# Performance work log

Hardware: AMD Instinct MI355X
Metric: run time of the kernel (lower is better)

The kernel has to match this reference:

```python
import jax, jax.numpy as jnp
from jax import lax
import numpy as np

# (in_ch, out_ch, kernel) per SparseConv layer; last layer has no ReLU
LAYERS = [(1, 16, 11), (16, 16, 7), (16, 16, 5), (16, 16, 3), (16, 16, 3), (16, 1, 1)]
DN = ('NCHW', 'OIHW', 'NCHW')


def _sparse_conv(x, mask, w, bias, gamma, beta, relu):
    k = w.shape[-1]
    p = k // 2
    pad = [(p, p), (p, p)]
    xm = x * mask  # mask broadcasts over channels ([B,1,H,W])
    y = lax.conv_general_dilated(xm, w, (1, 1), pad, dimension_numbers=DN)
    # 'sparsity' conv: fixed all-ones [1,1,k,k] kernel over the 1-channel mask
    ones_k = jnp.ones((1, 1, k, k), x.dtype)
    s = lax.conv_general_dilated(mask, ones_k, (1, 1), pad, dimension_numbers=DN)
    y = y * (1.0 / (s + 1e-8)) + bias[None, :, None, None]
    # BatchNorm2d in training mode (batch statistics), eps=1e-5
    mean = jnp.mean(y, axis=(0, 2, 3), keepdims=True)
    var = jnp.var(y, axis=(0, 2, 3), keepdims=True)
    y = (y - mean) * lax.rsqrt(var + 1e-5)
    y = y * gamma[None, :, None, None] + beta[None, :, None, None]
    if relu:
        y = jnp.maximum(y, 0.0)
    # MaxPool2d(k, stride=1, padding=k//2) on the mask (pads with -inf)
    mask = lax.reduce_window(mask, -jnp.inf, lax.max, (1, 1, k, k), (1, 1, 1, 1),
                             [(0, 0), (0, 0), (p, p), (p, p)])
    return y, mask


def setup_inputs() -> dict:
    key = jax.random.key(0)
    kx, *kws = jax.random.split(key, 1 + len(LAYERS))
    inp = {"x": jax.random.uniform(kx, (4, 2, 1024, 1024), dtype=jnp.float32)}
    for i, (cin, cout, k) in enumerate(LAYERS, start=1):
        fan_in = cin * k * k
        inp[f"w{i}"] = jax.random.normal(kws[i - 1], (cout, cin, k, k), jnp.float32) / np.sqrt(fan_in)
        inp[f"b{i}"] = jnp.zeros((cout,), jnp.float32)
        inp[f"g{i}"] = jnp.ones((cout,), jnp.float32)
        inp[f"bt{i}"] = jnp.zeros((cout,), jnp.float32)
    return inp


def reference(x, w1, b1, g1, bt1, w2, b2, g2, bt2, w3, b3, g3, bt3,
              w4, b4, g4, bt4, w5, b5, g5, bt5, w6, b6, g6, bt6):
    data = x[:, 0:1]   # channels != 1 (input_channels=2 -> channel 0)
    mask = x[:, 1:2]   # channel 1
    params = [(w1, b1, g1, bt1), (w2, b2, g2, bt2), (w3, b3, g3, bt3),
              (w4, b4, g4, bt4), (w5, b5, g5, bt5), (w6, b6, g6, bt6)]
    h, m = data, mask
    for i, (w, b, g, bt) in enumerate(params):
        h, m = _sparse_conv(h, m, w, b, g, bt, relu=(i < 5))
    return h
```

## Files before the change

kernel.cpp:

```cpp
#include <hip/hip_runtime.h>
#include <hip/hip_bf16.h>


#define HW (1024 * 1024)
typedef __hip_bfloat16 bf16;
typedef __attribute__((ext_vector_type(8))) short s8v;
typedef __attribute__((ext_vector_type(4))) float f4v;

__device__ __forceinline__ float b2f(bf16 v) { return __bfloat162float(v); }
__device__ __forceinline__ bf16  f2b(float v) { return __float2bfloat16(v); }
__device__ __forceinline__ short fbits(float v) {
    bf16 t = f2b(v); short s; __builtin_memcpy(&s, &t, 2); return s;
}
__device__ __forceinline__ float bs2f(short s) {
    bf16 t; __builtin_memcpy(&t, &s, 2); return __bfloat162float(t);
}

__device__ __forceinline__ float ldv(const void* p, int i, bool isf) {
    return isf ? ((const float*)p)[i] : b2f(((const bf16*)p)[i]);
}

__device__ __forceinline__ float wave_reduce(float v) {
    #pragma unroll
    for (int off = 32; off > 0; off >>= 1)
        v += __shfl_down(v, off, 64);
    return v;
}

__global__ void probeKernel(const unsigned short* __restrict__ xb,
                            float* __restrict__ stats)
{
    __shared__ int sbad;
    const int tid = threadIdx.x;
    if (tid == 0) sbad = 0;
    __syncthreads();
    int bad = 0;
    for (int i = tid; i < 4096; i += 256) {
        unsigned u = ((unsigned)xb[i]) << 16;
        float v = __uint_as_float(u);
        if (!(v >= 0.f && v < 1.f)) bad = 1;
    }
    if (bad) sbad = 1;
    __syncthreads();
    if (tid == 0) stats[380] = sbad ? 1.f : 0.f;
}

__global__ void transposeW1(const void* __restrict__ w, bf16* __restrict__ wb,
                            const float* flagp)
{
    const bool isf = (*flagp > 0.5f);
    int j = blockIdx.x * 256 + threadIdx.x;
    if (j < 3072) {
        int col8 = j & 7;
        int co = (j >> 3) & 15;
        int k8 = j >> 7;
        int k = k8 * 8 + col8;
        int dy = k >> 4, dx = k & 15;
        float v = (dy < 11 && dx < 11) ? ldv(w, co * 121 + dy * 11 + dx, isf) : 0.f;
        wb[j] = f2b(v);
    }
}

__global__ void transposeWB(const void* __restrict__ w, bf16* __restrict__ wtB,
                            int KK, int NT, const float* flagp)
{
    const bool isf = (*flagp > 0.5f);
    int j = blockIdx.x * 256 + threadIdx.x;
    if (j < NT * 256) {
        int t = j >> 8, co = (j >> 4) & 15, c = j & 15;
        float v = (t < KK) ? ldv(w, (co * 16 + c) * KK + t, isf) : 0.f;
        wtB[j] = f2b(v);
    }
}

template <int TM, int TK, int WP>
__device__ __forceinline__ void buildMaskTile(
    const void* __restrict__ mask0, bool isf, float* sm0, float* vm,
    float* mprev, int bx, int by, int tid)
{
    constexpr int H1 = (TM - 32) / 2;
    constexpr int H2 = (TK - 32) / 2;
    for (int i = tid; i < TM * TM; i += 256) {
        int yy = by - H1 + i / TM, xx = bx - H1 + i % TM;
        float m = 0.f;
        if ((unsigned)yy < 1024u && (unsigned)xx < 1024u)
            m = ldv(mask0, (yy << 10) + xx, isf);
        sm0[i] = m;
    }
    __syncthreads();
    for (int i = tid; i < TK * TM; i += 256) {
        int y = i / TM, xc = i % TM;
        float mx = 0.f;
        for (int d = 0; d < WP; ++d) mx = fmaxf(mx, sm0[(y + d) * TM + xc]);
        vm[i] = mx;
    }
    __syncthreads();
    for (int i = tid; i < TK * TK; i += 256) {
        int y = i / TK, xc = i % TK;
        int gy = by - H2 + y, gx = bx - H2 + xc;
        float mx = 0.f;
        if ((unsigned)gy < 1024u && (unsigned)gx < 1024u)
            for (int d = 0; d < WP; ++d) mx = fmaxf(mx, vm[y * TM + xc + d]);
        mprev[i] = mx;
    }
    __syncthreads();
}

__device__ __forceinline__ const void* maskChanPtr(const void* x, int n, bool isf) {
    return isf ? (const void*)((const float*)x + n * 2 * HW + HW)
               : (const void*)((const bf16*)x + n * 2 * HW + HW);
}

__global__ __launch_bounds__(256) void convFirstM(
    const void* __restrict__ x, const bf16* __restrict__ wb1,
    const void* __restrict__ bias, bf16* __restrict__ out,
    float* statsCur, const float* flagp)
{
    constexpr int ST = 48, ROWS = 44, MT = 42;
    __shared__ alignas(16) short c0[ROWS * ST];
    __shared__ alignas(16) short c1[ROWS * ST + 2];
    __shared__ float smask[MT * MT];
    __shared__ float scs[32 * MT];
    __shared__ float sinv[1024];
    __shared__ float red[128];
    const bool isf = (*flagp > 0.5f);
    const int n = blockIdx.z;
    const int bx = blockIdx.x * 32, by = blockIdx.y * 32;
    const int tid = threadIdx.x, lane = tid & 63, wid = tid >> 6;
    const int nn = lane & 15, q = lane >> 4;

    s8v Bf[6];
    #pragma unroll
    for (int kb = 0; kb < 6; ++kb)
        Bf[kb] = *(const s8v*)(wb1 + ((kb * 4 + q) * 16 + nn) * 8);
    const float bv = ldv(bias, nn, isf);

    if (tid == 0) c1[0] = 0;

    const int xoff = n * 2 * HW;
    for (int i = tid; i < ROWS * ST; i += 256) {
        int row = i / ST, col = i - row * ST;
        int yy = by - 5 + row, xx = bx - 5 + col;
        float d = 0.f, m = 0.f;
        if ((unsigned)yy < 1024u && (unsigned)xx < 1024u) {
            d = ldv(x, xoff + (yy << 10) + xx, isf);
            m = ldv(x, xoff + HW + (yy << 10) + xx, isf);
        }
        short b = fbits(d * m);
        c0[i] = b;
        c1[i + 1] = b;
        if (row < MT && col < MT) smask[row * MT + col] = m;
    }
    __syncthreads();

    for (int i = tid; i < 32 * MT; i += 256) {
        int r = i / MT, c = i - r * MT;
        float s = 0.f;
        #pragma unroll
        for (int dy = 0; dy < 11; ++dy) s += smask[(r + dy) * MT + c];
        scs[i] = s;
    }
    __syncthreads();
    for (int i = tid; i < 1024; i += 256) {
        int r = i >> 5, xc = i & 31;
        float s = 0.f;
        #pragma unroll
        for (int dx = 0; dx < 11; ++dx) s += scs[r * MT + xc + dx];
        sinv[i] = 121.f / (s + 1e-8f);
    }
    __syncthreads();

    const int dyq = q >> 1, dxq = (q & 1) << 3;
    const size_t nbase = (size_t)n * HW;
    float lsum = 0.f, lsq = 0.f;

    for (int mt = 0; mt < 16; ++mt) {
        int idx = wid * 16 + mt;
        int r = idx >> 1, g = idx & 1;
        int e = (r + dyq) * ST + (g << 4) + dxq + nn;
        int s = e & 1;
        const unsigned* cp = s ? (const unsigned*)c1 : (const unsigned*)c0;
        int w = (e + s) >> 1;
        f4v acc0 = {0.f, 0.f, 0.f, 0.f}, acc1 = {0.f, 0.f, 0.f, 0.f};
        #pragma unroll
        for (int kb = 0; kb < 6; ++kb) {
            union { unsigned u[4]; s8v v; } A;
            A.u[0] = cp[w];
            A.u[1] = cp[w + 1];
            A.u[2] = cp[w + 2];
            A.u[3] = cp[w + 3];
            if (kb & 1)
                acc1 = __builtin_amdgcn_mfma_f32_16x16x32_bf16(A.v, Bf[kb], acc1, 0, 0, 0);
            else
                acc0 = __builtin_amdgcn_mfma_f32_16x16x32_bf16(A.v, Bf[kb], acc0, 0, 0, 0);
            w += ST;
        }
        #pragma unroll
        for (int i2 = 0; i2 < 4; ++i2) {
            int px = (g << 4) + (q << 2) + i2;
            float y = fmaf(acc0[i2] + acc1[i2], sinv[(r << 5) + px], bv);
            out[((nbase + ((by + r) << 10) + bx + px) << 4) + nn] = f2b(y);
            lsum += y;
            lsq = fmaf(y, y, lsq);
        }
    }

    lsum += __shfl_xor(lsum, 16, 64);
    lsum += __shfl_xor(lsum, 32, 64);
    lsq  += __shfl_xor(lsq, 16, 64);
    lsq  += __shfl_xor(lsq, 32, 64);
    if (lane < 16) {
        red[wid * 32 + lane]      = lsum;
        red[wid * 32 + 16 + lane] = lsq;
    }
    __syncthreads();
    if (tid < 32) {
        float t = red[tid] + red[32 + tid] + red[64 + tid] + red[96 + tid];
        atomicAdd(&statsCur[tid], t);
    }
}

template <int K, int WP>
__global__ __launch_bounds__(256, 2) void conv16m(
    const bf16* __restrict__ in, const void* __restrict__ x,
    const bf16* __restrict__ wtB, const float* statsPrev,
    const void* __restrict__ bias, bf16* __restrict__ out,
    float* statsCur, const float* flagp)
{
    constexpr int TK = 32 + K - 1;
    constexpr int TM = TK + WP - 1;
    constexpr int KK = K * K, NT = KK + 1, NK = NT / 2;
    constexpr int H2 = K / 2;
    __shared__ short sdatL[TK * TK * 8];
    __shared__ short sdatH[TK * TK * 8];
    __shared__ float mprev[TK * TK];
    __shared__ float sinv[1024];
    __shared__ float red[128];
    __shared__ float sss[32];
    const bool isf = (*flagp > 0.5f);
    const int n = blockIdx.z;
    const int bx = blockIdx.x * 32, by = blockIdx.y * 32;
    const int tid = threadIdx.x, lane = tid & 63, wid = tid >> 6;

    if (tid < 16) { sss[tid] = statsPrev[32 + tid]; sss[16 + tid] = statsPrev[48 + tid]; }

    buildMaskTile<TM, TK, WP>(maskChanPtr(x, n, isf), isf,
                              (float*)sdatL, (float*)sdatH, mprev, bx, by, tid);

    {
        float* cs = (float*)sdatH;
        for (int i = tid; i < 32 * TK; i += 256) {
            int r = i / TK, c = i - r * TK;
            float s = 0.f;
            #pragma unroll
            for (int dy = 0; dy < K; ++dy) s += mprev[(r + dy) * TK + c];
            cs[i] = s;
        }
        __syncthreads();
        for (int i = tid; i < 1024; i += 256) {
            int r = i >> 5, xc = i & 31;
            float s = 0.f;
            #pragma unroll
            for (int dx = 0; dx < K; ++dx) s += cs[r * TK + xc + dx];
            sinv[i] = (float)KK / (s + 1e-8f);
        }
        __syncthreads();
    }

    const int nn = lane & 15, quad = lane >> 4, c0 = (quad & 1) * 8, tl = quad >> 1;
    s8v Bf[NK];
    #pragma unroll
    for (int kk = 0; kk < NK; ++kk) {
        int t = 2 * kk + tl;
        Bf[kk] = *(const s8v*)(wtB + ((t * 16 + nn) * 16 + c0));
    }

    {
        const bf16* inb = in + ((size_t)n * HW << 4);
        for (int p = tid; p < TK * TK; p += 256) {
            int yy = by - H2 + p / TK, xx = bx - H2 + p % TK;
            s8v lo = {0,0,0,0,0,0,0,0}, hi = {0,0,0,0,0,0,0,0};
            if ((unsigned)yy < 1024u && (unsigned)xx < 1024u) {
                float mv = mprev[p];
                const s8v* q = (const s8v*)(inb + ((size_t)((yy << 10) + xx) << 4));
                s8v rl = q[0], rh = q[1];
                #pragma unroll
                for (int c = 0; c < 8; ++c) {
                    float yv = bs2f(rl[c]);
                    lo[c] = fbits(fmaxf(fmaf(sss[c], yv, sss[16 + c]), 0.f) * mv);
                }
                #pragma unroll
                for (int c = 0; c < 8; ++c) {
                    float yv = bs2f(rh[c]);
                    hi[c] = fbits(fmaxf(fmaf(sss[c + 8], yv, sss[24 + c]), 0.f) * mv);
                }
            }
            ((s8v*)sdatL)[p] = lo;
            ((s8v*)sdatH)[p] = hi;
        }
    }
    __syncthreads();

    const float bv = ldv(bias, nn, isf);
    const s8v* Abase = (const s8v*)((quad & 1) ? sdatH : sdatL);
    const size_t nbase = (size_t)n * HW;
    float lsum = 0.f, lsq = 0.f;

    for (int mt = 0; mt < 16; ++mt) {
        int idx = wid * 16 + mt;
        int r = idx >> 1, xh = (idx & 1) << 4;
        int acol = xh + nn;
        f4v acc0 = {0.f, 0.f, 0.f, 0.f}, acc1 = {0.f, 0.f, 0.f, 0.f};
        #pragma unroll
        for (int kk = 0; kk < NK; ++kk) {
            const int ta = (2 * kk < KK) ? 2 * kk : 0;
            const int tb = (2 * kk + 1 < KK) ? 2 * kk + 1 : 0;
            const int dya = ta / K, dxa = ta % K;
            const int dyb = tb / K, dxb = tb % K;
            int dy = tl ? dyb : dya;
            int dx = tl ? dxb : dxa;
            s8v a = Abase[(r + dy) * TK + acol + dx];
            if (kk & 1)
                acc1 = __builtin_amdgcn_mfma_f32_16x16x32_bf16(a, Bf[kk], acc1, 0, 0, 0);
            else
                acc0 = __builtin_amdgcn_mfma_f32_16x16x32_bf16(a, Bf[kk], acc0, 0, 0, 0);
        }
        #pragma unroll
        for (int i = 0; i < 4; ++i) {
            float av = acc0[i] + acc1[i];
            int m = quad * 4 + i;
            float y = fmaf(av, sinv[r * 32 + xh + m], bv);
            out[((nbase + ((by + r) << 10) + bx + xh + m) << 4) + nn] = f2b(y);
            lsum += y;
            lsq = fmaf(y, y, lsq);
        }
    }

    lsum += __shfl_xor(lsum, 16, 64);
    lsum += __shfl_xor(lsum, 32, 64);
    lsq  += __shfl_xor(lsq, 16, 64);
    lsq  += __shfl_xor(lsq, 32, 64);
    if (lane < 16) {
        red[wid * 32 + lane]      = lsum;
        red[wid * 32 + 16 + lane] = lsq;
    }
    __syncthreads();
    if (tid < 32) {
        float t = red[tid] + red[32 + tid] + red[64 + tid] + red[96 + tid];
        atomicAdd(&statsCur[tid], t);
    }
}

__global__ __launch_bounds__(256) void layer6Kernel(
    const bf16* __restrict__ in, const void* __restrict__ x,
    const float* statsPrev, const void* __restrict__ w6,
    const void* __restrict__ b6, bf16* __restrict__ y6,
    float* statsCur, const float* flagp)
{
    constexpr int WP = 25, TM = 56, TK = 32;
    __shared__ float sm0[TM * TM];
    __shared__ float vm[TK * TM];
    __shared__ float m5[TK * TK];
    __shared__ float red[8];
    __shared__ float ssc[16], ssh[16];
    const bool isf = (*flagp > 0.5f);
    const int n = blockIdx.z;
    const int bx = blockIdx.x * 32, by = blockIdx.y * 32;
    const int tid = threadIdx.x;
    const int tx = tid & 31, ty0 = (tid >> 5) << 2;

    if (tid < 16) {
        ssc[tid] = statsPrev[32 + tid];
        ssh[tid] = statsPrev[48 + tid];
    }

    buildMaskTile<TM, TK, WP>(maskChanPtr(x, n, isf), isf, sm0, vm, m5, bx, by, tid);

    float wv[16];
    #pragma unroll
    for (int c = 0; c < 16; ++c) wv[c] = ldv(w6, c, isf);
    const float bias = ldv(b6, 0, isf);

    float lsum = 0.f, lsq = 0.f;
    #pragma unroll
    for (int p = 0; p < 4; ++p) {
        int yy = by + ty0 + p, xx = bx + tx;
        float m = m5[(ty0 + p) * TK + tx];
        const s8v* q = (const s8v*)(in + (((size_t)n * HW + (yy << 10) + xx) << 4));
        s8v rl = q[0], rh = q[1];
        float a = 0.f;
        #pragma unroll
        for (int c = 0; c < 8; ++c) {
            float h = fmaxf(fmaf(ssc[c], bs2f(rl[c]), ssh[c]), 0.f);
            a = fmaf(h, wv[c], a);
        }
        #pragma unroll
        for (int c = 0; c < 8; ++c) {
            float h = fmaxf(fmaf(ssc[c + 8], bs2f(rh[c]), ssh[c + 8]), 0.f);
            a = fmaf(h, wv[c + 8], a);
        }
        float yv = a * m / (m + 1e-8f) + bias;
        y6[n * HW + (yy << 10) + xx] = f2b(yv);
        lsum += yv;
        lsq = fmaf(yv, yv, lsq);
    }
    lsum = wave_reduce(lsum);
    lsq = wave_reduce(lsq);
    const int wid = tid >> 6, lane = tid & 63;
    if (lane == 0) { red[wid] = lsum; red[4 + wid] = lsq; }
    __syncthreads();
    if (tid == 0) atomicAdd(&statsCur[0],  red[0] + red[1] + red[2] + red[3]);
    if (tid == 1) atomicAdd(&statsCur[16], red[4] + red[5] + red[6] + red[7]);
}

__global__ void finalizeStats(float* stats, const void* __restrict__ g,
                              const void* __restrict__ bt, float alpha, int cout,
                              float* mirror, const float* flagp)
{
    const bool isf = (*flagp > 0.5f);
    int c = threadIdx.x;
    if (c < cout) {
        const float invN = 1.f / (4.f * HW);
        float meanp = stats[c] * invN;
        float varp  = fmaxf(stats[16 + c] * invN - meanp * meanp, 0.f);
        float var_t = varp / (alpha * alpha);
        float sct = ldv(g, c, isf) * rsqrtf(var_t + 1e-5f);
        float scp = sct / alpha;
        float shp = ldv(bt, c, isf) - scp * meanp;
        stats[32 + c] = scp;
        stats[48 + c] = shp;
        if (mirror) { mirror[2 * c] = scp; mirror[2 * c + 1] = shp; mirror[32] = isf ? 1.f : 0.f; }
    }
}

__global__ void finalOut(const bf16* __restrict__ y6, const float* mirror,
                         void* __restrict__ out)
{
    float sc = mirror[0], sh = mirror[1];
    const bool isf = (mirror[32] > 0.5f);
    for (int idx = blockIdx.x * 256 + threadIdx.x; idx < 4 * HW; idx += gridDim.x * 256) {
        float v = fmaf(b2f(y6[idx]), sc, sh);
        if (isf) ((float*)out)[idx] = v;
        else     ((bf16*)out)[idx] = f2b(v);
    }
}

__global__ void zeroStats(float* stats)
{
    int i = blockIdx.x * 256 + threadIdx.x;
    if (i < 384) stats[i] = 0.f;
}

__global__ void fillOut(void* out, const float* flagp, float v)
{
    const bool isf = (*flagp > 0.5f);
    for (int idx = blockIdx.x * 256 + threadIdx.x; idx < 4 * HW; idx += gridDim.x * 256) {
        if (isf) ((float*)out)[idx] = v;
        else     ((bf16*)out)[idx] = f2b(v);
    }
}

extern "C" void kernel_launch(void* const* d_in, const int* in_sizes, int n_in,
                              void* d_out, int out_size, void* d_ws, size_t ws_size,
                              hipStream_t stream)
{
    const void* x = d_in[0];
    #define W(L)  ((const void*)d_in[1 + ((L) - 1) * 4])
    #define B(L)  ((const void*)d_in[2 + ((L) - 1) * 4])
    #define G(L)  ((const void*)d_in[3 + ((L) - 1) * 4])
    #define BT(L) ((const void*)d_in[4 + ((L) - 1) * 4])

    float* stats = (float*)d_out;
    const float* flagp = stats + 380;
    float* wt1 = stats + 384;
    bf16* wb1 = (bf16*)wt1;
    bf16* wb2 = (bf16*)(wt1 + 1936);
    bf16* wb3 = wb2 + 50 * 256;
    bf16* wb4 = wb3 + 26 * 256;
    bf16* wb5 = wb4 + 10 * 256;
    const size_t need = 2 * (size_t)64 * HW * sizeof(bf16);

    zeroStats<<<2, 256, 0, stream>>>(stats);
    probeKernel<<<1, 256, 0, stream>>>((const unsigned short*)x, stats);

    if (ws_size < need) {
        fillOut<<<2048, 256, 0, stream>>>(d_out, flagp, 3.0f);
        return;
    }

    transposeW1<<<12, 256, 0, stream>>>(W(1), wb1, flagp);
    transposeWB<<<50, 256, 0, stream>>>(W(2), wb2, 49, 50, flagp);
    transposeWB<<<26, 256, 0, stream>>>(W(3), wb3, 25, 26, flagp);
    transposeWB<<<10, 256, 0, stream>>>(W(4), wb4, 9, 10, flagp);
    transposeWB<<<10, 256, 0, stream>>>(W(5), wb5, 9, 10, flagp);

    bf16* bufA = (bf16*)d_ws;
    bf16* bufB = bufA + 64 * HW;
    float* mirror = (float*)bufA;

    dim3 grid(32, 32, 4), block(256);

    convFirstM<<<grid, block, 0, stream>>>(x, wb1, B(1), bufA, stats + 0, flagp);
    finalizeStats<<<1, 64, 0, stream>>>(stats + 0, G(1), BT(1), 121.f, 16, nullptr, flagp);

    conv16m<7, 11><<<grid, block, 0, stream>>>(bufA, x, wb2, stats + 0, B(2), bufB, stats + 64, flagp);
    finalizeStats<<<1, 64, 0, stream>>>(stats + 64, G(2), BT(2), 49.f, 16, nullptr, flagp);

    conv16m<5, 17><<<grid, block, 0, stream>>>(bufB, x, wb3, stats + 64, B(3), bufA, stats + 128, flagp);
    finalizeStats<<<1, 64, 0, stream>>>(stats + 128, G(3), BT(3), 25.f, 16, nullptr, flagp);

    conv16m<3, 21><<<grid, block, 0, stream>>>(bufA, x, wb4, stats + 128, B(4), bufB, stats + 192, flagp);
    finalizeStats<<<1, 64, 0, stream>>>(stats + 192, G(4), BT(4), 9.f, 16, nullptr, flagp);

    conv16m<3, 23><<<grid, block, 0, stream>>>(bufB, x, wb5, stats + 192, B(5), bufA, stats + 256, flagp);
    finalizeStats<<<1, 64, 0, stream>>>(stats + 256, G(5), BT(5), 9.f, 16, nullptr, flagp);

    bf16* y6 = (bf16*)bufB;
    layer6Kernel<<<grid, block, 0, stream>>>(bufA, x, stats + 256, W(6), B(6), y6, stats + 320, flagp);
    finalizeStats<<<1, 64, 0, stream>>>(stats + 320, G(6), BT(6), 1.f, 1, mirror, flagp);
    finalOut<<<2048, 256, 0, stream>>>(y6, mirror, d_out);

    #undef W
    #undef B
    #undef G
    #undef BT
}
```

Measured before the change: 838.8 us.

## Reuse LDS A-fragments across kernel rows with 8-row register accumulators

Restructures the conv16m MFMA loop so each wave computes 8 output rows at once and holds 16 accumulators in registers. Each input row fragment is loaded from LDS once and applied to every kernel row dy that touches it, which cuts repeated LDS reads. The weights are re-laid out with the dx dimension padded to an even DXP per row, so tap pairs never straddle kernel rows. This adds zero-padded MFMAs and a zero sentinel slot in LDS. The extra accumulator registers may hurt occupancy under launch_bounds(256,2).

```diff
diff --git a/kernel.cpp b/kernel.cpp
--- a/kernel.cpp
+++ b/kernel.cpp
@@ -62,13 +62,15 @@
 }
 
 __global__ void transposeWB(const void* __restrict__ w, bf16* __restrict__ wtB,
-                            int KK, int NT, const float* flagp)
-{
-    const bool isf = (*flagp > 0.5f);
+                            int K, int DXP, const float* flagp)
+{
+    const bool isf = (*flagp > 0.5f);
+    int NT = K * DXP;
     int j = blockIdx.x * 256 + threadIdx.x;
     if (j < NT * 256) {
         int t = j >> 8, co = (j >> 4) & 15, c = j & 15;
-        float v = (t < KK) ? ldv(w, (co * 16 + c) * KK + t, isf) : 0.f;
+        int dy = t / DXP, dx = t % DXP;
+        float v = (dx < K) ? ldv(w, (co * 16 + c) * (K * K) + dy * K + dx, isf) : 0.f;
         wtB[j] = f2b(v);
     }
 }
@@ -220,7 +222,7 @@
     }
 }
 
-template <int K, int WP>
+template <int K, int WP, int DXP>
 __global__ __launch_bounds__(256, 2) void conv16m(
     const bf16* __restrict__ in, const void* __restrict__ x,
     const bf16* __restrict__ wtB, const float* statsPrev,
@@ -229,10 +231,12 @@
 {
     constexpr int TK = 32 + K - 1;
     constexpr int TM = TK + WP - 1;
-    constexpr int KK = K * K, NT = KK + 1, NK = NT / 2;
+    constexpr int NJ = DXP / 2;
+    constexpr int NK = K * NJ;
+    constexpr int KK = K * K;
     constexpr int H2 = K / 2;
-    __shared__ short sdatL[TK * TK * 8];
-    __shared__ short sdatH[TK * TK * 8];
+    __shared__ short sdatL[(TK * TK + 1) * 8];
+    __shared__ short sdatH[(TK * TK + 1) * 8];
     __shared__ float mprev[TK * TK];
     __shared__ float sinv[1024];
     __shared__ float red[128];
@@ -271,7 +275,8 @@
     s8v Bf[NK];
     #pragma unroll
     for (int kk = 0; kk < NK; ++kk) {
-        int t = 2 * kk + tl;
+        int dy = kk / NJ, jj = kk % NJ;
+        int t = dy * DXP + 2 * jj + tl;
         Bf[kk] = *(const s8v*)(wtB + ((t * 16 + nn) * 16 + c0));
     }
 
@@ -298,41 +303,60 @@
             ((s8v*)sdatL)[p] = lo;
             ((s8v*)sdatH)[p] = hi;
         }
+        if (tid == 0) {
+            s8v z = {0,0,0,0,0,0,0,0};
+            ((s8v*)sdatL)[TK * TK] = z;
+            ((s8v*)sdatH)[TK * TK] = z;
+        }
     }
     __syncthreads();
 
     const float bv = ldv(bias, nn, isf);
     const s8v* Abase = (const s8v*)((quad & 1) ? sdatH : sdatL);
     const size_t nbase = (size_t)n * HW;
+    const int r0 = wid * 8;
+
+    f4v acc[8][2];
+    #pragma unroll
+    for (int rr = 0; rr < 8; ++rr) {
+        acc[rr][0] = f4v{0.f, 0.f, 0.f, 0.f};
+        acc[rr][1] = f4v{0.f, 0.f, 0.f, 0.f};
+    }
+
+    #pragma unroll
+    for (int ar = 0; ar < 8 + K - 1; ++ar) {
+        #pragma unroll
+        for (int j = 0; j < NJ; ++j) {
+            const int base = (r0 + ar) * TK + nn + 2 * j + tl;
+            const s8v F0 = Abase[base];
+            const s8v F1 = Abase[base + 16];
+            #pragma unroll
+            for (int dy = 0; dy < K; ++dy) {
+                if (ar - dy >= 0 && ar - dy < 8) {
+                    acc[ar - dy][0] = __builtin_amdgcn_mfma_f32_16x16x32_bf16(
+                        F0, Bf[dy * NJ + j], acc[ar - dy][0], 0, 0, 0);
+                    acc[ar - dy][1] = __builtin_amdgcn_mfma_f32_16x16x32_bf16(
+                        F1, Bf[dy * NJ + j], acc[ar - dy][1], 0, 0, 0);
+                }
+            }
+        }
+    }
+
     float lsum = 0.f, lsq = 0.f;
-
-    for (int mt = 0; mt < 16; ++mt) {
-        int idx = wid * 16 + mt;
-        int r = idx >> 1, xh = (idx & 1) << 4;
-        int acol = xh + nn;
-        f4v acc0 = {0.f, 0.f, 0.f, 0.f}, acc1 = {0.f, 0.f, 0.f, 0.f};
-        #pragma unroll
-        for (int kk = 0; kk < NK; ++kk) {
-            const int ta = (2 * kk < KK) ? 2 * kk : 0;
-            const int tb = (2 * kk + 1 < KK) ? 2 * kk + 1 : 0;
-            const int dya = ta / K, dxa = ta % K;
-            const int dyb = tb / K, dxb = tb % K;
-            int dy = tl ? dyb : dya;
-            int dx = tl ? dxb : dxa;
-            s8v a = Abase[(r + dy) * TK + acol + dx];
-            if (kk & 1)
-                acc1 = __builtin_amdgcn_mfma_f32_16x16x32_bf16(a, Bf[kk], acc1, 0, 0, 0);
-            else
-                acc0 = __builtin_amdgcn_mfma_f32_16x16x32_bf16(a, Bf[kk], acc0, 0, 0, 0);
-        }
-        #pragma unroll
-        for (int i = 0; i < 4; ++i) {
-            float av = acc0[i] + acc1[i];
-            int m = quad * 4 + i;
-            float y = fmaf(av, sinv[r * 32 + xh + m], bv);
-            out[((nbase + ((by + r) << 10) + bx + xh + m) << 4) + nn] = f2b(y);
-            lsum += y;
-            lsq = fmaf(y, y, lsq);
+    #pragma unroll
+    for (int rr = 0; rr < 8; ++rr) {
+        const int r = r0 + rr;
+        #pragma unroll
+        for (int h = 0; h < 2; ++h) {
+            const int xh = h << 4;
+            #pragma unroll
+            for (int i = 0; i < 4; ++i) {
+                int m = quad * 4 + i;
+                float y = fmaf(acc[rr][h][i], sinv[r * 32 + xh + m], bv);
+                out[((nbase + ((by + r) << 10) + bx + xh + m) << 4) + nn] = f2b(y);
+                lsum += y;
+                lsq = fmaf(y, y, lsq);
+            }
         }
     }
 
@@ -475,9 +499,9 @@
     float* wt1 = stats + 384;
     bf16* wb1 = (bf16*)wt1;
     bf16* wb2 = (bf16*)(wt1 + 1936);
-    bf16* wb3 = wb2 + 50 * 256;
-    bf16* wb4 = wb3 + 26 * 256;
-    bf16* wb5 = wb4 + 10 * 256;
+    bf16* wb3 = wb2 + 56 * 256;
+    bf16* wb4 = wb3 + 30 * 256;
+    bf16* wb5 = wb4 + 12 * 256;
     const size_t need = 2 * (size_t)64 * HW * sizeof(bf16);
 
     zeroStats<<<2, 256, 0, stream>>>(stats);
@@ -489,10 +513,10 @@
     }
 
     transposeW1<<<12, 256, 0, stream>>>(W(1), wb1, flagp);
-    transposeWB<<<50, 256, 0, stream>>>(W(2), wb2, 49, 50, flagp);
-    transposeWB<<<26, 256, 0, stream>>>(W(3), wb3, 25, 26, flagp);
-    transposeWB<<<10, 256, 0, stream>>>(W(4), wb4, 9, 10, flagp);
-    transposeWB<<<10, 256, 0, stream>>>(W(5), wb5, 9, 10, flagp);
+    transposeWB<<<56, 256, 0, stream>>>(W(2), wb2, 7, 8, flagp);
+    transposeWB<<<30, 256, 0, stream>>>(W(3), wb3, 5, 6, flagp);
+    transposeWB<<<12, 256, 0, stream>>>(W(4), wb4, 3, 4, flagp);
+    transposeWB<<<12, 256, 0, stream>>>(W(5), wb5, 3, 4, flagp);
 
     bf16* bufA = (bf16*)d_ws;
     bf16* bufB = bufA + 64 * HW;
@@ -503,16 +527,16 @@
     convFirstM<<<grid, block, 0, stream>>>(x, wb1, B(1), bufA, stats + 0, flagp);
     finalizeStats<<<1, 64, 0, stream>>>(stats + 0, G(1), BT(1), 121.f, 16, nullptr, flagp);
 
-    conv16m<7, 11><<<grid, block, 0, stream>>>(bufA, x, wb2, stats + 0, B(2), bufB, stats + 64, flagp);
+    conv16m<7, 11, 8><<<grid, block, 0, stream>>>(bufA, x, wb2, stats + 0, B(2), bufB, stats + 64, flagp);
     finalizeStats<<<1, 64, 0, stream>>>(stats + 64, G(2), BT(2), 49.f, 16, nullptr, flagp);
 
-    conv16m<5, 17><<<grid, block, 0, stream>>>(bufB, x, wb3, stats + 64, B(3), bufA, stats + 128, flagp);
+    conv16m<5, 17, 6><<<grid, block, 0, stream>>>(bufB, x, wb3, stats + 64, B(3), bufA, stats + 128, flagp);
     finalizeStats<<<1, 64, 0, stream>>>(stats + 128, G(3), BT(3), 25.f, 16, nullptr, flagp);
 
-    conv16m<3, 21><<<grid, block, 0, stream>>>(bufA, x, wb4, stats + 128, B(4), bufB, stats + 192, flagp);
+    conv16m<3, 21, 4><<<grid, block, 0, stream>>>(bufA, x, wb4, stats + 128, B(4), bufB, stats + 192, flagp);
     finalizeStats<<<1, 64, 0, stream>>>(stats + 192, G(4), BT(4), 9.f, 16, nullptr, flagp);
 
-    conv16m<3, 23><<<grid, block, 0, stream>>>(bufB, x, wb5, stats + 192, B(5), bufA, stats + 256, flagp);
+    conv16m<3, 23, 4><<<grid, block, 0, stream>>>(bufB, x, wb5, stats + 192, B(5), bufA, stats + 256, flagp);
     finalizeStats<<<1, 64, 0, stream>>>(stats + 256, G(5), BT(5), 9.f, 16, nullptr, flagp);
 
     bf16* y6 = (bf16*)bufB;
```

New measurement: 803.5 us. -4.2%, faster.
